# Optimization experiments

Hardware: AMD Instinct MI355X
Metric: run time of the kernel (lower is better)

The kernel has to match this reference:

```python
import jax, jax.numpy as jnp
import numpy as np

N, D, H = 8192, 1280, 16
K = D // H          # head_dim = 80
S = 16              # number of packed segments
L = N // S          # tokens per segment = 512
SCALE = K ** -0.5


def rotate_half(x):
    x1, x2 = jnp.split(x, 2, axis=-1)
    return jnp.concatenate([-x2, x1], axis=-1)


def setup_inputs() -> dict:
    key = jax.random.key(0)
    ks = jax.random.split(key, 4)
    # RoPE tables over head_dim, shared by all heads
    inv_freq = 1.0 / (10000.0 ** (jnp.arange(0, K, 2, dtype=jnp.float32) / K))
    freqs = jnp.outer(jnp.arange(N, dtype=jnp.float32), inv_freq)  # [N, K/2]
    emb = jnp.concatenate([freqs, freqs], axis=-1)                 # [N, K]
    return {
        "hidden_ND": jax.random.normal(ks[0], (N, D), jnp.float32),
        "cu_seqlens": jnp.arange(S + 1, dtype=jnp.int32) * L,      # equal-length segments
        "cos_NK": jnp.cos(emb),
        "sin_NK": jnp.sin(emb),
        "qkv_w": jax.random.normal(ks[1], (D, 3 * D), jnp.float32) * (D ** -0.5),
        "qkv_b": jnp.zeros((3 * D,), jnp.float32),
        "proj_w": jax.random.normal(ks[2], (D, D), jnp.float32) * (D ** -0.5),
        "proj_b": jnp.zeros((D,), jnp.float32),
    }


def reference(hidden_ND, cu_seqlens, cos_NK, sin_NK, qkv_w, qkv_b, proj_w, proj_b):
    n = hidden_ND.shape[0]
    qkv = (hidden_ND @ qkv_w + qkv_b).reshape(n, 3, H, K)
    q, k, v = qkv[:, 0], qkv[:, 1], qkv[:, 2]          # each [N, H, K]
    cos = cos_NK[:, None, :]
    sin = sin_NK[:, None, :]
    q = q * cos + rotate_half(q) * sin
    k = k * cos + rotate_half(k) * sin
    # Block-diagonal attention over equal-length segments defined by cu_seqlens.
    num_seqs = cu_seqlens.shape[0] - 1
    seg_len = n // num_seqs
    qs = q.reshape(num_seqs, seg_len, H, K)
    ks_ = k.reshape(num_seqs, seg_len, H, K)
    vs = v.reshape(num_seqs, seg_len, H, K)
    logits = jnp.einsum('slhk,smhk->shlm', qs, ks_) * SCALE   # [S, H, L, L]
    w = jax.nn.softmax(logits.astype(jnp.float32), axis=-1).astype(logits.dtype)
    out = jnp.einsum('shlm,smhk->slhk', w, vs).reshape(n, H * K)
    return out @ proj_w + proj_b
```

## Files before the change

### kernel.cpp

```cpp
#include <hip/hip_runtime.h>

#define LOG2E 1.44269504088896340736f
#define ATT_SCALE 0.11180339887498949f

typedef _Float16 half8 __attribute__((ext_vector_type(8)));
typedef _Float16 half4v __attribute__((ext_vector_type(4)));
typedef __fp16 fp16x2 __attribute__((ext_vector_type(2)));
typedef float f32x4 __attribute__((ext_vector_type(4)));

#define MFMA(a, b, c) __builtin_amdgcn_mfma_f32_16x16x32_f16((a), (b), (c), 0, 0, 0)

__device__ __forceinline__ void async16(const _Float16* g, _Float16* l) {
  __builtin_amdgcn_global_load_lds(
      (const __attribute__((address_space(1))) unsigned int*)g,
      (__attribute__((address_space(3))) unsigned int*)l,
      16, 0, 0);
}

#define FENCE() asm volatile("" ::: "memory")
#define PHB()                                   \
  do {                                          \
    FENCE();                                    \
    __builtin_amdgcn_s_barrier();               \
    FENCE();                                    \
  } while (0)

__global__ __launch_bounds__(256) void cvt_k(const float* __restrict__ in,
                                             _Float16* __restrict__ out, int n4) {
  int i = blockIdx.x * 256 + threadIdx.x;
  if (i < n4) {
    f32x4 v = ((const f32x4*)in)[i];
    half4v hv;
    hv[0] = (_Float16)v[0]; hv[1] = (_Float16)v[1];
    hv[2] = (_Float16)v[2]; hv[3] = (_Float16)v[3];
    ((half4v*)out)[i] = hv;
  }
}

__global__ __launch_bounds__(256) void transpose_cvt_k(const float* __restrict__ in,
                                                       _Float16* __restrict__ out,
                                                       int R, int C) {
  __shared__ float tile[32][33];
  const int tx = threadIdx.x & 31, ty = threadIdx.x >> 5;
  const int c0 = blockIdx.x * 32, r0 = blockIdx.y * 32;
#pragma unroll
  for (int i = 0; i < 32; i += 8)
    tile[ty + i][tx] = in[(size_t)(r0 + ty + i) * C + c0 + tx];
  __syncthreads();
#pragma unroll
  for (int i = 0; i < 32; i += 8)
    out[(size_t)(c0 + ty + i) * R + r0 + tx] = (_Float16)tile[tx][ty + i];
}

__global__ __launch_bounds__(512, 2) void gemm256_k(const _Float16* __restrict__ A,
                                                    const _Float16* __restrict__ BT,
                                                    const float* __restrict__ bias,
                                                    _Float16* __restrict__ Qf,
                                                    _Float16* __restrict__ Kf,
                                                    _Float16* __restrict__ VTf) {
  __shared__ _Float16 sA[2][2][128 * 64];
  __shared__ _Float16 sB[2][2][128 * 64];
  const int tid = threadIdx.x;
  const int wave = tid >> 6, lane = tid & 63;
  const int quad = lane >> 4, l16 = lane & 15;
  const int wm = wave >> 2, wn = wave & 3;
  const int bh = wn >> 1, brb = (wn & 1) * 64;
  const int KD = 1280, NT = 20;

  const int id = blockIdx.x;
  const int xcd = id & 7;
  const int qq = (id >> 3) & 3;
  const int tn = id >> 5;
  const int tm = xcd * 4 + qq;
  const int m0 = tm * 256, n0 = tn * 256;

  f32x4 acc[8][4] = {};

  auto stageA = [&](int buf, int half, int kt) {
#pragma unroll
    for (int c = 0; c < 2; ++c) {
      const int s = c * 512 + wave * 64 + lane;
      const int row = s >> 3;
      const int lg = (s & 7) ^ (row & 7);
      async16(A + (size_t)(m0 + half * 128 + row) * KD + kt * 64 + lg * 8,
              &sA[buf][half][(size_t)(c * 512 + wave * 64) * 8]);
    }
  };
  auto stageB = [&](int buf, int half, int kt) {
#pragma unroll
    for (int c = 0; c < 2; ++c) {
      const int s = c * 512 + wave * 64 + lane;
      const int row = s >> 3;
      const int lg = (s & 7) ^ (row & 7);
      async16(BT + (size_t)(n0 + half * 128 + row) * KD + kt * 64 + lg * 8,
              &sB[buf][half][(size_t)(c * 512 + wave * 64) * 8]);
    }
  };
  auto ldA = [&](half8* af, const _Float16* hp, int rh) {
#pragma unroll
    for (int i = 0; i < 4; ++i)
#pragma unroll
      for (int kk = 0; kk < 2; ++kk) {
        const int lrow = rh * 64 + i * 16 + l16;
        const int pg = (kk * 4 + quad) ^ (l16 & 7);
        af[i * 2 + kk] = *(const half8*)(hp + lrow * 64 + pg * 8);
      }
  };
  auto ldB = [&](half8* bf, const _Float16* hp, int ch) {
#pragma unroll
    for (int j = 0; j < 2; ++j)
#pragma unroll
      for (int kk = 0; kk < 2; ++kk) {
        const int brow = brb + ch * 32 + j * 16 + l16;
        const int pg = (kk * 4 + quad) ^ (l16 & 7);
        bf[j * 2 + kk] = *(const half8*)(hp + brow * 64 + pg * 8);
      }
  };
  auto mmaq = [&](int r, int c, const half8* af, const half8* bf) {
#pragma unroll
    for (int i = 0; i < 4; ++i)
#pragma unroll
      for (int j = 0; j < 2; ++j)
#pragma unroll
        for (int kk = 0; kk < 2; ++kk)
          acc[r * 4 + i][c * 2 + j] =
              MFMA(af[i * 2 + kk], bf[j * 2 + kk], acc[r * 4 + i][c * 2 + j]);
  };

  stageA(0, 0, 0); stageA(0, 1, 0);
  stageB(0, 0, 0); stageB(0, 1, 0);
  stageB(1, 0, 1); stageB(1, 1, 1);
  asm volatile("s_waitcnt vmcnt(4)" ::: "memory");

  half8 af[8], bf0[4], bf1[4];
#pragma unroll 2
  for (int t = 0; t < NT; ++t) {
    const int buf = t & 1;
    const _Float16* aH = &sA[0][0][0] + buf * (2 * 128 * 64) + wm * (128 * 64);
    const _Float16* bH = &sB[0][0][0] + buf * (2 * 128 * 64) + bh * (128 * 64);

    PHB();
    ldA(af, aH, 0);
    ldB(bf0, bH, 0);
    if (t + 1 < NT) stageA(buf ^ 1, 0, t + 1);
    __builtin_amdgcn_s_setprio(1);
    mmaq(0, 0, af, bf0);
    __builtin_amdgcn_s_setprio(0);

    PHB();
    ldB(bf1, bH, 1);
    if (t + 1 < NT) stageA(buf ^ 1, 1, t + 1);
    __builtin_amdgcn_s_setprio(1);
    mmaq(0, 1, af, bf1);
    __builtin_amdgcn_s_setprio(0);

    PHB();
    ldA(af, aH, 1);
    if (t + 2 < NT) stageB(buf, 0, t + 2);
    __builtin_amdgcn_s_setprio(1);
    mmaq(1, 1, af, bf1);
    __builtin_amdgcn_s_setprio(0);

    PHB();
    if (t + 2 < NT) stageB(buf, 1, t + 2);
    if (t == NT - 2)
      asm volatile("s_waitcnt vmcnt(0)" ::: "memory");
    else if (t < NT - 2)
      asm volatile("s_waitcnt vmcnt(4)" ::: "memory");
    __builtin_amdgcn_s_setprio(1);
    mmaq(1, 0, af, bf0);
    __builtin_amdgcn_s_setprio(0);
  }

#pragma unroll
  for (int ridx = 0; ridx < 8; ++ridx) {
#pragma unroll
    for (int cidx = 0; cidx < 4; ++cidx) {
      const int col = n0 + wn * 64 + cidx * 16 + l16;
      const float bv = bias[col];
      const int rowb = m0 + wm * 128 + ridx * 16 + quad * 4;
      const int which = col / 1280;
      const int rem = col - which * 1280;
      const int h = rem / 80;
      const int kk = rem - h * 80;
#pragma unroll
      for (int r = 0; r < 4; ++r) {
        const float v = acc[ridx][cidx][r] + bv;
        const int mrow = rowb + r;
        const int s = mrow >> 9, l = mrow & 511;
        const int shh = s * 16 + h;
        if (which == 0)
          Qf[((size_t)shh * 512 + l) * 96 + kk] = (_Float16)v;
        else if (which == 1)
          Kf[((size_t)shh * 512 + l) * 96 + kk] = (_Float16)v;
        else
          VTf[((size_t)shh * 80 + kk) * 512 + l] = (_Float16)v;
      }
    }
  }
}

__global__ __launch_bounds__(256) void gemm_k(const _Float16* __restrict__ A,
                                              const _Float16* __restrict__ BT,
                                              const float* __restrict__ bias,
                                              float* __restrict__ Out) {
  __shared__ _Float16 sA[128 * 32];
  __shared__ _Float16 sB[128 * 32];
  const int tid = threadIdx.x;
  const int wave = tid >> 6, lane = tid & 63;
  const int quad = lane >> 4, l16 = lane & 15;
  const int m0 = blockIdx.x * 128;
  const int n0 = blockIdx.y * 128;
  const int mw = (wave & 1) * 64, nw = (wave >> 1) * 64;
  const int KD = 1280;

  const int srcg = (lane & 3) ^ ((lane >> 3) & 3);
  const int rg = (quad ^ ((l16 >> 1) & 3)) * 8;

  f32x4 acc[4][4] = {};

  for (int kt = 0; kt < KD; kt += 32) {
#pragma unroll
    for (int c = 0; c < 2; ++c) {
      const int j = wave * 2 + c;
      const int row = j * 16 + (lane >> 2);
      async16(A + (size_t)(m0 + row) * KD + kt + srcg * 8, &sA[j * 512]);
      async16(BT + (size_t)(n0 + row) * KD + kt + srcg * 8, &sB[j * 512]);
    }
    __syncthreads();
    half8 af[4], bf[4];
#pragma unroll
    for (int i = 0; i < 4; ++i) {
      af[i] = *(const half8*)&sA[(mw + i * 16 + l16) * 32 + rg];
      bf[i] = *(const half8*)&sB[(nw + i * 16 + l16) * 32 + rg];
    }
#pragma unroll
    for (int i = 0; i < 4; ++i)
#pragma unroll
      for (int j2 = 0; j2 < 4; ++j2)
        acc[i][j2] = MFMA(af[i], bf[j2], acc[i][j2]);
    __syncthreads();
  }

#pragma unroll
  for (int i = 0; i < 4; ++i) {
#pragma unroll
    for (int j2 = 0; j2 < 4; ++j2) {
      const int col = n0 + nw + j2 * 16 + l16;
      const float bv = bias[col];
      const int rowb = m0 + mw + i * 16 + quad * 4;
#pragma unroll
      for (int r = 0; r < 4; ++r)
        Out[(size_t)(rowb + r) * 1280 + col] = acc[i][j2][r] + bv;
    }
  }
}

__global__ __launch_bounds__(256) void rope_k(_Float16* __restrict__ Qf,
                                              _Float16* __restrict__ Kf,
                                              const float* __restrict__ cosNK,
                                              const float* __restrict__ sinNK) {
  const int gid = blockIdx.x * 256 + threadIdx.x;
  const int j = gid & 63;
  const int row = gid >> 6;
  const int qk = row >> 17;
  const int r = row & 131071;
  _Float16* buf = qk ? Kf : Qf;
  const int l = r & 511;
  const int s = r >> 13;
  const int t = s * 512 + l;
  const size_t base = (size_t)r * 96;
  if (j < 40) {
    const float v1 = (float)buf[base + j];
    const float v2 = (float)buf[base + j + 40];
    const float c1 = cosNK[t * 80 + j], s1 = sinNK[t * 80 + j];
    const float c2 = cosNK[t * 80 + j + 40], s2 = sinNK[t * 80 + j + 40];
    buf[base + j] = (_Float16)(v1 * c1 - v2 * s1);
    buf[base + j + 40] = (_Float16)(v2 * c2 + v1 * s2);
  } else if (j < 56) {
    buf[base + 40 + j] = (_Float16)0.f;
  }
}

__global__ __launch_bounds__(256) void attn_k(const _Float16* __restrict__ Qf,
                                              const _Float16* __restrict__ Kf,
                                              const _Float16* __restrict__ VTf,
                                              _Float16* __restrict__ attnA) {
  __shared__ _Float16 sP[128 * 72];
  __shared__ _Float16 sK[64 * 104];
  __shared__ _Float16 sV[96 * 72];
  const int tid = threadIdx.x;
  const int wave = tid >> 6, lane = tid & 63;
  const int quad = lane >> 4, l16 = lane & 15;
  const int shh = blockIdx.x;
  const int qt = blockIdx.y;
  const int h = shh & 15;
  const int s = shh >> 4;

  const _Float16* Qb = Qf + ((size_t)shh * 512 + qt * 128) * 96;
  const _Float16* Kb0 = Kf + (size_t)shh * 512 * 96;
  const _Float16* Vb0 = VTf + (size_t)shh * 80 * 512;

  const _Float16 c1h = (_Float16)(ATT_SCALE * LOG2E);
  half8 qf[2][3];
#pragma unroll
  for (int rt = 0; rt < 2; ++rt)
#pragma unroll
    for (int ks = 0; ks < 3; ++ks) {
      half8 t = *(const half8*)(Qb + (size_t)(wave * 32 + rt * 16 + l16) * 96 +
                                ks * 32 + quad * 8);
#pragma unroll
      for (int e = 0; e < 8; ++e) t[e] *= c1h;
      qf[rt][ks] = t;
    }

  for (int idx = tid; idx < 16 * 72; idx += 256) sV[80 * 72 + idx] = (_Float16)1.f;

  f32x4 o[2][6] = {};

  for (int kc = 0; kc < 8; ++kc) {
    __syncthreads();
    const _Float16* Kb = Kb0 + (size_t)kc * 64 * 96;
#pragma unroll
    for (int c = 0; c < 4; ++c) {
      const int j = wave + 4 * c;
      if (j < 13) {
        const int off = j * 1024 + lane * 16;
        const int krow = off / 208;
        const int kcol = off - krow * 208;
        if (kcol < 192)
          async16(Kb + (size_t)krow * 96 + (kcol >> 1), &sK[j * 512]);
      }
    }
#pragma unroll
    for (int c = 0; c < 3; ++c) {
      const int j = wave + 4 * c;
      const int off = j * 1024 + lane * 16;
      const int vrow = off / 144;
      const int colb = off - vrow * 144;
      if (vrow < 80 && colb < 128)
        async16(Vb0 + (size_t)vrow * 512 + kc * 64 + (colb >> 1), &sV[j * 512]);
    }
    __syncthreads();

    f32x4 sacc[2][4] = {};
#pragma unroll
    for (int mt = 0; mt < 4; ++mt) {
#pragma unroll
      for (int ks = 0; ks < 3; ++ks) {
        half8 kb = *(const half8*)&sK[(mt * 16 + l16) * 104 + ks * 32 + quad * 8];
        sacc[0][mt] = MFMA(kb, qf[0][ks], sacc[0][mt]);
        sacc[1][mt] = MFMA(kb, qf[1][ks], sacc[1][mt]);
      }
    }

#pragma unroll
    for (int rt = 0; rt < 2; ++rt) {
#pragma unroll
      for (int mt = 0; mt < 4; ++mt) {
        union { fp16x2 h2[2]; half4v h4; } u;
        u.h2[0] = __builtin_amdgcn_cvt_pkrtz(
            __builtin_amdgcn_exp2f(sacc[rt][mt][0]),
            __builtin_amdgcn_exp2f(sacc[rt][mt][1]));
        u.h2[1] = __builtin_amdgcn_cvt_pkrtz(
            __builtin_amdgcn_exp2f(sacc[rt][mt][2]),
            __builtin_amdgcn_exp2f(sacc[rt][mt][3]));
        *(half4v*)&sP[(wave * 32 + rt * 16 + l16) * 72 + mt * 16 + quad * 4] = u.h4;
      }
    }

#pragma unroll
    for (int ks = 0; ks < 2; ++ks) {
      half8 pa[2];
      pa[0] = *(const half8*)&sP[(wave * 32 + 0 + l16) * 72 + ks * 32 + quad * 8];
      pa[1] = *(const half8*)&sP[(wave * 32 + 16 + l16) * 72 + ks * 32 + quad * 8];
#pragma unroll
      for (int ft = 0; ft < 6; ++ft) {
        half8 vb = *(const half8*)&sV[(ft * 16 + l16) * 72 + ks * 32 + quad * 8];
        o[0][ft] = MFMA(pa[0], vb, o[0][ft]);
        o[1][ft] = MFMA(pa[1], vb, o[1][ft]);
      }
    }
  }

#pragma unroll
  for (int rt = 0; rt < 2; ++rt) {
#pragma unroll
    for (int r = 0; r < 4; ++r) {
      const float inv = 1.0f / o[rt][5][r];
      const int token = s * 512 + qt * 128 + wave * 32 + rt * 16 + quad * 4 + r;
#pragma unroll
      for (int ft = 0; ft < 5; ++ft)
        attnA[(size_t)token * 1280 + h * 80 + ft * 16 + l16] =
            (_Float16)(o[rt][ft][r] * inv);
    }
  }
}

extern "C" void kernel_launch(void* const* d_in, const int* in_sizes, int n_in,
                              void* d_out, int out_size, void* d_ws, size_t ws_size,
                              hipStream_t stream) {
  (void)in_sizes; (void)n_in; (void)out_size; (void)ws_size;
  const float* hidden = (const float*)d_in[0];
  const float* cosNK = (const float*)d_in[2];
  const float* sinNK = (const float*)d_in[3];
  const float* qkv_w = (const float*)d_in[4];
  const float* qkv_b = (const float*)d_in[5];
  const float* proj_w = (const float*)d_in[6];
  const float* proj_b = (const float*)d_in[7];
  float* out = (float*)d_out;

  char* ws = (char*)d_ws;
  _Float16* hA    = (_Float16*)(ws);
  _Float16* wT    = (_Float16*)(ws + 20971520);
  _Float16* projT = (_Float16*)(ws + 30801920);
  _Float16* Qf    = (_Float16*)(ws + 34078720);
  _Float16* Kf    = (_Float16*)(ws + 59244544);
  _Float16* VTf   = (_Float16*)(ws + 84410368);
  _Float16* attnA = (_Float16*)(ws + 105381888);

  cvt_k<<<10240, 256, 0, stream>>>(hidden, hA, 2621440);
  transpose_cvt_k<<<dim3(120, 40), 256, 0, stream>>>(qkv_w, wT, 1280, 3840);
  transpose_cvt_k<<<dim3(40, 40), 256, 0, stream>>>(proj_w, projT, 1280, 1280);
  gemm256_k<<<480, 512, 0, stream>>>(hA, wT, qkv_b, Qf, Kf, VTf);
  rope_k<<<65536, 256, 0, stream>>>(Qf, Kf, cosNK, sinNK);
  attn_k<<<dim3(256, 4), 256, 0, stream>>>(Qf, Kf, VTf, attnA);
  gemm_k<<<dim3(64, 10), 256, 0, stream>>>(attnA, projT, proj_b, out);
}
```

Before: 354.0 us.

## Double-buffer output projection GEMM with larger tiles and vectorize RoPE kernel

The output projection GEMM moves to 256x128 tiles with BK=64, double-buffered LDS staging via async global-to-LDS loads, XOR swizzling, and a four-phase schedule that overlaps prefetch with MFMA. The goal is to hide global load latency and raise data reuse per tile. Separately, the RoPE kernel switches from one element per thread with many idle lanes to four elements per thread using vector loads and stores, with far fewer blocks. This adds LDS pressure and hand-tuned vmcnt waits that must match the load count exactly.

```diff
diff --git a/kernel.cpp b/kernel.cpp
--- a/kernel.cpp
+++ b/kernel.cpp
@@ -204,54 +204,124 @@
                                               const _Float16* __restrict__ BT,
                                               const float* __restrict__ bias,
                                               float* __restrict__ Out) {
-  __shared__ _Float16 sA[128 * 32];
-  __shared__ _Float16 sB[128 * 32];
+  __shared__ _Float16 sA[2][2][128 * 64];
+  __shared__ _Float16 sB[2][2][64 * 64];
   const int tid = threadIdx.x;
   const int wave = tid >> 6, lane = tid & 63;
   const int quad = lane >> 4, l16 = lane & 15;
-  const int m0 = blockIdx.x * 128;
+  const int wm = wave >> 1, wn = wave & 1;
+  const int KD = 1280, NT = 20;
+
+  const int m0 = blockIdx.x * 256;
   const int n0 = blockIdx.y * 128;
-  const int mw = (wave & 1) * 64, nw = (wave >> 1) * 64;
-  const int KD = 1280;
-
-  const int srcg = (lane & 3) ^ ((lane >> 3) & 3);
-  const int rg = (quad ^ ((l16 >> 1) & 3)) * 8;
-
-  f32x4 acc[4][4] = {};
-
-  for (int kt = 0; kt < KD; kt += 32) {
-#pragma unroll
-    for (int c = 0; c < 2; ++c) {
-      const int j = wave * 2 + c;
-      const int row = j * 16 + (lane >> 2);
-      async16(A + (size_t)(m0 + row) * KD + kt + srcg * 8, &sA[j * 512]);
-      async16(BT + (size_t)(n0 + row) * KD + kt + srcg * 8, &sB[j * 512]);
-    }
-    __syncthreads();
-    half8 af[4], bf[4];
-#pragma unroll
-    for (int i = 0; i < 4; ++i) {
-      af[i] = *(const half8*)&sA[(mw + i * 16 + l16) * 32 + rg];
-      bf[i] = *(const half8*)&sB[(nw + i * 16 + l16) * 32 + rg];
-    }
+
+  f32x4 acc[8][4] = {};
+
+  auto stageA = [&](int buf, int half, int kt) {
+#pragma unroll
+    for (int c = 0; c < 4; ++c) {
+      const int s = c * 256 + tid;
+      const int row = s >> 3;
+      const int lg = (s & 7) ^ (row & 7);
+      async16(A + (size_t)(m0 + half * 128 + row) * KD + kt * 64 + lg * 8,
+              &sA[buf][half][(size_t)(c * 256 + wave * 64) * 8]);
+    }
+  };
+  auto stageB = [&](int buf, int kt) {
+#pragma unroll
+    for (int c = 0; c < 4; ++c) {
+      const int s = c * 256 + tid;
+      const int row = s >> 3;
+      const int lg = (s & 7) ^ (row & 7);
+      async16(BT + (size_t)(n0 + row) * KD + kt * 64 + lg * 8,
+              &sB[buf][0][(size_t)(c * 256 + wave * 64) * 8]);
+    }
+  };
+  auto ldA = [&](half8* af, const _Float16* hp, int rh) {
 #pragma unroll
     for (int i = 0; i < 4; ++i)
 #pragma unroll
-      for (int j2 = 0; j2 < 4; ++j2)
-        acc[i][j2] = MFMA(af[i], bf[j2], acc[i][j2]);
-    __syncthreads();
-  }
-
-#pragma unroll
-  for (int i = 0; i < 4; ++i) {
-#pragma unroll
-    for (int j2 = 0; j2 < 4; ++j2) {
-      const int col = n0 + nw + j2 * 16 + l16;
+      for (int kk = 0; kk < 2; ++kk) {
+        const int lrow = rh * 64 + i * 16 + l16;
+        const int pg = (kk * 4 + quad) ^ (l16 & 7);
+        af[i * 2 + kk] = *(const half8*)(hp + lrow * 64 + pg * 8);
+      }
+  };
+  auto ldB = [&](half8* bf, const _Float16* hp, int ch) {
+#pragma unroll
+    for (int j = 0; j < 2; ++j)
+#pragma unroll
+      for (int kk = 0; kk < 2; ++kk) {
+        const int brow = ch * 32 + j * 16 + l16;
+        const int pg = (kk * 4 + quad) ^ (l16 & 7);
+        bf[j * 2 + kk] = *(const half8*)(hp + brow * 64 + pg * 8);
+      }
+  };
+  auto mmaq = [&](int r, int c, const half8* af, const half8* bf) {
+#pragma unroll
+    for (int i = 0; i < 4; ++i)
+#pragma unroll
+      for (int j = 0; j < 2; ++j)
+#pragma unroll
+        for (int kk = 0; kk < 2; ++kk)
+          acc[r * 4 + i][c * 2 + j] =
+              MFMA(af[i * 2 + kk], bf[j * 2 + kk], acc[r * 4 + i][c * 2 + j]);
+  };
+
+  stageA(0, 0, 0); stageA(0, 1, 0);
+  stageB(0, 0);
+  stageB(1, 1);
+  asm volatile("s_waitcnt vmcnt(4)" ::: "memory");
+
+  half8 af[8], bf0[4], bf1[4];
+#pragma unroll 2
+  for (int t = 0; t < NT; ++t) {
+    const int buf = t & 1;
+    const _Float16* aH = &sA[0][0][0] + buf * (2 * 128 * 64) + wm * (128 * 64);
+    const _Float16* bH = &sB[0][0][0] + buf * (2 * 64 * 64) + wn * (64 * 64);
+
+    PHB();
+    ldA(af, aH, 0);
+    ldB(bf0, bH, 0);
+    if (t + 1 < NT) stageA(buf ^ 1, 0, t + 1);
+    __builtin_amdgcn_s_setprio(1);
+    mmaq(0, 0, af, bf0);
+    __builtin_amdgcn_s_setprio(0);
+
+    PHB();
+    ldB(bf1, bH, 1);
+    if (t + 1 < NT) stageA(buf ^ 1, 1, t + 1);
+    __builtin_amdgcn_s_setprio(1);
+    mmaq(0, 1, af, bf1);
+    __builtin_amdgcn_s_setprio(0);
+
+    PHB();
+    ldA(af, aH, 1);
+    if (t + 2 < NT) stageB(buf, t + 2);
+    __builtin_amdgcn_s_setprio(1);
+    mmaq(1, 1, af, bf1);
+    __builtin_amdgcn_s_setprio(0);
+
+    PHB();
+    if (t == NT - 2)
+      asm volatile("s_waitcnt vmcnt(0)" ::: "memory");
+    else if (t < NT - 2)
+      asm volatile("s_waitcnt vmcnt(4)" ::: "memory");
+    __builtin_amdgcn_s_setprio(1);
+    mmaq(1, 0, af, bf0);
+    __builtin_amdgcn_s_setprio(0);
+  }
+
+#pragma unroll
+  for (int ridx = 0; ridx < 8; ++ridx) {
+#pragma unroll
+    for (int cidx = 0; cidx < 4; ++cidx) {
+      const int col = n0 + wn * 64 + cidx * 16 + l16;
       const float bv = bias[col];
-      const int rowb = m0 + mw + i * 16 + quad * 4;
+      const int rowb = m0 + wm * 128 + ridx * 16 + quad * 4;
 #pragma unroll
       for (int r = 0; r < 4; ++r)
-        Out[(size_t)(rowb + r) * 1280 + col] = acc[i][j2][r] + bv;
+        Out[(size_t)(rowb + r) * 1280 + col] = acc[ridx][cidx][r] + bv;
     }
   }
 }
@@ -261,8 +331,8 @@
                                               const float* __restrict__ cosNK,
                                               const float* __restrict__ sinNK) {
   const int gid = blockIdx.x * 256 + threadIdx.x;
-  const int j = gid & 63;
-  const int row = gid >> 6;
+  const int jt = gid % 10;
+  const int row = gid / 10;
   const int qk = row >> 17;
   const int r = row & 131071;
   _Float16* buf = qk ? Kf : Qf;
@@ -270,15 +340,26 @@
   const int s = r >> 13;
   const int t = s * 512 + l;
   const size_t base = (size_t)r * 96;
-  if (j < 40) {
-    const float v1 = (float)buf[base + j];
-    const float v2 = (float)buf[base + j + 40];
-    const float c1 = cosNK[t * 80 + j], s1 = sinNK[t * 80 + j];
-    const float c2 = cosNK[t * 80 + j + 40], s2 = sinNK[t * 80 + j + 40];
-    buf[base + j] = (_Float16)(v1 * c1 - v2 * s1);
-    buf[base + j + 40] = (_Float16)(v2 * c2 + v1 * s2);
-  } else if (j < 56) {
-    buf[base + 40 + j] = (_Float16)0.f;
+  const int j0 = jt * 4;
+
+  half4v v1 = *(const half4v*)(buf + base + j0);
+  half4v v2 = *(const half4v*)(buf + base + 40 + j0);
+  f32x4 c1 = *(const f32x4*)(cosNK + (size_t)t * 80 + j0);
+  f32x4 s1 = *(const f32x4*)(sinNK + (size_t)t * 80 + j0);
+  f32x4 c2 = *(const f32x4*)(cosNK + (size_t)t * 80 + 40 + j0);
+  f32x4 s2 = *(const f32x4*)(sinNK + (size_t)t * 80 + 40 + j0);
+  half4v o1, o2;
+#pragma unroll
+  for (int e = 0; e < 4; ++e) {
+    const float a = (float)v1[e], b = (float)v2[e];
+    o1[e] = (_Float16)(a * c1[e] - b * s1[e]);
+    o2[e] = (_Float16)(b * c2[e] + a * s2[e]);
+  }
+  *(half4v*)(buf + base + j0) = o1;
+  *(half4v*)(buf + base + 40 + j0) = o2;
+  if (jt < 2) {
+    half8 z = {};
+    *(half8*)(buf + base + 80 + jt * 8) = z;
   }
 }
 
@@ -423,7 +504,7 @@
   transpose_cvt_k<<<dim3(120, 40), 256, 0, stream>>>(qkv_w, wT, 1280, 3840);
   transpose_cvt_k<<<dim3(40, 40), 256, 0, stream>>>(proj_w, projT, 1280, 1280);
   gemm256_k<<<480, 512, 0, stream>>>(hA, wT, qkv_b, Qf, Kf, VTf);
-  rope_k<<<65536, 256, 0, stream>>>(Qf, Kf, cosNK, sinNK);
+  rope_k<<<10240, 256, 0, stream>>>(Qf, Kf, cosNK, sinNK);
   attn_k<<<dim3(256, 4), 256, 0, stream>>>(Qf, Kf, VTf, attnA);
-  gemm_k<<<dim3(64, 10), 256, 0, stream>>>(attnA, projT, proj_b, out);
-}
+  gemm_k<<<dim3(32, 10), 256, 0, stream>>>(attnA, projT, proj_b, out);
+}
```

Result: no change. 358.8 us (+1.4%).
